# Kernel optimization log

Measured on AMD Instinct MI355X. Metric: run time of the kernel, lower is better.

## Reference

```python
import jax, jax.numpy as jnp
import numpy as np

B, N, E = 8, 50000, 800000
IN_DIM, OUT_DIM = 64, 64


def setup_inputs() -> dict:
    key = jax.random.key(0)
    k_x, k_src, k_dst, k_ws, k_bs, k_wn, k_bn = jax.random.split(key, 7)
    x = jax.random.normal(k_x, (B, N, IN_DIM), dtype=jnp.float32)
    src = jax.random.randint(k_src, (E,), 0, N, dtype=jnp.int64)
    dst = jax.random.randint(k_dst, (E,), 0, N, dtype=jnp.int64)
    edge_index = jnp.stack([src, dst], axis=1)  # (E, 2)
    # nn.Linear init: U(-1/sqrt(in_dim), 1/sqrt(in_dim))
    bound = 1.0 / np.sqrt(IN_DIM)
    W_self = jax.random.uniform(k_ws, (OUT_DIM, IN_DIM), jnp.float32, -bound, bound)
    b_self = jax.random.uniform(k_bs, (OUT_DIM,), jnp.float32, -bound, bound)
    W_neigh = jax.random.uniform(k_wn, (OUT_DIM, IN_DIM), jnp.float32, -bound, bound)
    b_neigh = jax.random.uniform(k_bn, (OUT_DIM,), jnp.float32, -bound, bound)
    return {"x": x, "edge_index": edge_index, "W_self": W_self, "b_self": b_self,
            "W_neigh": W_neigh, "b_neigh": b_neigh}


def reference(x, edge_index, W_self, b_self, W_neigh, b_neigh):
    # x: (B, N, D); edge_index: (E, 2) [src, dst], shared topology across batch
    src = edge_index[:, 0]
    dst = edge_index[:, 1]
    # scatter-add neighbor aggregation, vectorized over batch
    agg = jnp.zeros_like(x).at[:, dst].add(x[:, src])  # (B, N, D)
    h_self = jnp.einsum('bnd,od->bno', x, W_self) + b_self
    h_neigh = jnp.einsum('bnd,od->bno', agg, W_neigh) + b_neigh
    return jax.nn.relu(h_self + h_neigh)
```

## Files before the change

kernel.cpp:

```cpp
#include <hip/hip_runtime.h>

#define Bn 8
#define Nn 50000
#define En 800000
#define Dd 64
#define CAP 64

typedef __attribute__((ext_vector_type(8))) unsigned short ushort8;
typedef __attribute__((ext_vector_type(8))) __bf16 bf16x8;
typedef __attribute__((ext_vector_type(4))) float floatx4;

__device__ __forceinline__ unsigned short f2bf(float f) {
  unsigned int u = __builtin_bit_cast(unsigned int, f);
  u = (u + 0x7FFFu + ((u >> 16) & 1u)) >> 16;
  return (unsigned short)u;
}

__device__ __forceinline__ int swz(int row, int byte_in_row) {
  return (row * 256 + byte_in_row) ^ ((row & 7) << 4);
}

__global__ __launch_bounds__(256) void k_fconv(const float* __restrict__ x,
                                               unsigned short* __restrict__ xb,
                                               const int* __restrict__ ei,
                                               int* __restrict__ deg,
                                               unsigned short* __restrict__ bucket,
                                               const float* __restrict__ Ws,
                                               const float* __restrict__ Wn,
                                               const float* __restrict__ bs,
                                               const float* __restrict__ bn,
                                               unsigned short* __restrict__ Wb,
                                               float* __restrict__ bb) {
  const size_t gid = (size_t)blockIdx.x * 256 + threadIdx.x;
  const size_t i = gid * 4;
  const float4 v = *(const float4*)(x + i);
  ushort4 o;
  o.x = f2bf(v.x); o.y = f2bf(v.y); o.z = f2bf(v.z); o.w = f2bf(v.w);
  *(ushort4*)(xb + i) = o;
  if ((gid & 7) == 0) {
    const size_t e = gid >> 3;
    const int2 ep = *(const int2*)(ei + 2 * e);
    const int p = atomicAdd(&deg[ep.y], 1);
    if (p < CAP) bucket[((size_t)ep.y << 6) + p] = (unsigned short)ep.x;
  }
  if (gid < 1024) {
    const int f = (int)gid >> 6, ln = (int)gid & 63;
    const int t = f >> 2, k = f & 3;
    const int col = ln & 15, quad = ln >> 4;
    const int orow = t * 16 + col;
    const int kd = k * 32 + quad * 8;
    const float* wsrc = (kd < 64) ? (Ws + orow * 64 + kd) : (Wn + orow * 64 + (kd - 64));
    ushort8 u;
    #pragma unroll
    for (int j = 0; j < 8; ++j) u[j] = f2bf(wsrc[j]);
    *(ushort8*)(Wb + gid * 8) = u;
  }
  if (gid < 64) bb[gid] = bs[gid] + bn[gid];
}

__global__ __launch_bounds__(256, 8) void k_main(
    const unsigned short* __restrict__ xb, const unsigned short* __restrict__ bucket,
    const int* __restrict__ deg, const unsigned short* __restrict__ Wb,
    const float* __restrict__ bb, float* __restrict__ out) {
  __shared__ __align__(16) unsigned short A[64 * 128];

  const int tid = threadIdx.x;
  const int b = blockIdx.x & 7;
  const int node0 = (blockIdx.x >> 3) * 64;
  const int wave = tid >> 6;
  const int lane = tid & 63;
  char* Ac = (char*)A;

  const int slot = lane >> 3;
  const int li = lane & 7;
  const size_t xb_base = (size_t)b * Nn * Dd + (size_t)(li * 8);

  for (int g = 0; g < 2; ++g) {
    const int nl = wave * 16 + g * 8 + slot;
    const int node = node0 + nl;
    float acc[8] = {0.f, 0.f, 0.f, 0.f, 0.f, 0.f, 0.f, 0.f};
    if (node < Nn) {
      const uint4 sv = *(const uint4*)(xb + xb_base + (size_t)node * Dd);
      const int cnt = min(deg[node], CAP);
      const unsigned short* bkt = bucket + (node << 6);
      const int nch = (cnt + 7) >> 3;
      for (int c = 0; c < nch; ++c) {
        const uint4 e = *(const uint4*)(bkt + c * 8);
        const unsigned int ew[4] = {e.x, e.y, e.z, e.w};
        #pragma unroll
        for (int t = 0; t < 8; ++t) {
          unsigned int s = (ew[t >> 1] >> ((t & 1) * 16)) & 0xFFFFu;
          const float m = (s < (unsigned)Nn) ? 1.0f : 0.0f;
          s = min(s, (unsigned)(Nn - 1));
          const uint4 v = *(const uint4*)(xb + xb_base + (size_t)s * Dd);
          const unsigned int w[4] = {v.x, v.y, v.z, v.w};
          #pragma unroll
          for (int j = 0; j < 4; ++j) {
            acc[2 * j]     = fmaf(m, __builtin_bit_cast(float, w[j] << 16), acc[2 * j]);
            acc[2 * j + 1] = fmaf(m, __builtin_bit_cast(float, w[j] & 0xFFFF0000u), acc[2 * j + 1]);
          }
        }
      }
      *(uint4*)(Ac + swz(nl, li * 16)) = sv;
    } else {
      *(uint4*)(Ac + swz(nl, li * 16)) = make_uint4(0, 0, 0, 0);
    }
    ushort8 av;
    #pragma unroll
    for (int j = 0; j < 8; ++j) av[j] = f2bf(acc[j]);
    *(ushort8*)(Ac + swz(nl, 128 + li * 16)) = av;
  }

  const int col = lane & 15;
  const int quad = lane >> 4;
  bf16x8 af[4];
  {
    const int row = wave * 16 + col;
    #pragma unroll
    for (int k = 0; k < 4; ++k)
      af[k] = __builtin_bit_cast(bf16x8, *(const ushort8*)(Ac + swz(row, quad * 16 + k * 64)));
  }
  #pragma unroll
  for (int t = 0; t < 4; ++t) {
    floatx4 acc = {0.f, 0.f, 0.f, 0.f};
    #pragma unroll
    for (int k = 0; k < 4; ++k) {
      bf16x8 bf = __builtin_bit_cast(bf16x8, *(const ushort8*)(Wb + ((t * 4 + k) * 64 + lane) * 8));
      acc = __builtin_amdgcn_mfma_f32_16x16x32_bf16(af[k], bf, acc, 0, 0, 0);
    }
    const float bv = bb[t * 16 + col];
    #pragma unroll
    for (int r = 0; r < 4; ++r) {
      const int node = node0 + wave * 16 + quad * 4 + r;
      if (node < Nn) {
        float v = acc[r] + bv;
        out[((size_t)b * Nn + node) * Dd + t * 16 + col] = v > 0.f ? v : 0.f;
      }
    }
  }
}

#define OFF_XB 0ull
#define OFF_DEG 51200000ull
#define OFF_BKT 51400000ull
#define OFF_WB 57800000ull
#define OFF_BB 57816384ull
#define WS_NEED 57816640ull

extern "C" void kernel_launch(void* const* d_in, const int* in_sizes, int n_in,
                              void* d_out, int out_size, void* d_ws,
                              size_t ws_size, hipStream_t stream) {
  const float* x = (const float*)d_in[0];
  const int* ei = (const int*)d_in[1];
  const float* Ws = (const float*)d_in[2];
  const float* bs = (const float*)d_in[3];
  const float* Wn = (const float*)d_in[4];
  const float* bn = (const float*)d_in[5];
  float* out = (float*)d_out;

  if (ws_size < WS_NEED) return;

  char* ws = (char*)d_ws;
  unsigned short* xb = (unsigned short*)(ws + OFF_XB);
  int* deg = (int*)(ws + OFF_DEG);
  unsigned short* bucket = (unsigned short*)(ws + OFF_BKT);
  unsigned short* Wb = (unsigned short*)(ws + OFF_WB);
  float* bb = (float*)(ws + OFF_BB);

  hipMemsetAsync(deg, 0, Nn * sizeof(int), stream);
  hipMemsetAsync(bucket, 0xFF, (size_t)Nn * CAP * sizeof(unsigned short), stream);
  k_fconv<<<(Bn * Nn * Dd / 4) / 256, 256, 0, stream>>>(x, xb, ei, deg, bucket, Ws, Wn, bs, bn, Wb, bb);
  const int ntiles = (Nn + 63) / 64;
  k_main<<<ntiles * Bn, 256, 0, stream>>>(xb, bucket, deg, Wb, bb, out);
}
```

Before: 344.2 us.

## Interleave two nodes' gathers with batched loads and drop bucket memset

The gather loop now processes both nodes a thread owns together, issuing 16 independent row loads before accumulating and prefetching the next bucket chunk, so more memory requests are in flight per thread. Validity is now taken from the per-node count instead of a sentinel value, which makes the 6.4MB bucket memset unnecessary, so it is removed. Launch bounds drop from 8 to 3 blocks per SM to give room for the larger register footprint. The cost is lower occupancy, and both nodes run for the larger of their two chunk counts.

```diff
diff --git a/kernel.cpp b/kernel.cpp
--- a/kernel.cpp
+++ b/kernel.cpp
@@ -58,7 +58,7 @@
   if (gid < 64) bb[gid] = bs[gid] + bn[gid];
 }
 
-__global__ __launch_bounds__(256, 8) void k_main(
+__global__ __launch_bounds__(256, 3) void k_main(
     const unsigned short* __restrict__ xb, const unsigned short* __restrict__ bucket,
     const int* __restrict__ deg, const unsigned short* __restrict__ Wb,
     const float* __restrict__ bb, float* __restrict__ out) {
@@ -75,41 +75,89 @@
   const int li = lane & 7;
   const size_t xb_base = (size_t)b * Nn * Dd + (size_t)(li * 8);
 
-  for (int g = 0; g < 2; ++g) {
-    const int nl = wave * 16 + g * 8 + slot;
-    const int node = node0 + nl;
-    float acc[8] = {0.f, 0.f, 0.f, 0.f, 0.f, 0.f, 0.f, 0.f};
-    if (node < Nn) {
-      const uint4 sv = *(const uint4*)(xb + xb_base + (size_t)node * Dd);
-      const int cnt = min(deg[node], CAP);
-      const unsigned short* bkt = bucket + (node << 6);
-      const int nch = (cnt + 7) >> 3;
-      for (int c = 0; c < nch; ++c) {
-        const uint4 e = *(const uint4*)(bkt + c * 8);
-        const unsigned int ew[4] = {e.x, e.y, e.z, e.w};
-        #pragma unroll
-        for (int t = 0; t < 8; ++t) {
-          unsigned int s = (ew[t >> 1] >> ((t & 1) * 16)) & 0xFFFFu;
-          const float m = (s < (unsigned)Nn) ? 1.0f : 0.0f;
-          s = min(s, (unsigned)(Nn - 1));
-          const uint4 v = *(const uint4*)(xb + xb_base + (size_t)s * Dd);
-          const unsigned int w[4] = {v.x, v.y, v.z, v.w};
-          #pragma unroll
-          for (int j = 0; j < 4; ++j) {
-            acc[2 * j]     = fmaf(m, __builtin_bit_cast(float, w[j] << 16), acc[2 * j]);
-            acc[2 * j + 1] = fmaf(m, __builtin_bit_cast(float, w[j] & 0xFFFF0000u), acc[2 * j + 1]);
-          }
-        }
+  const int nl0 = wave * 16 + slot;
+  const int nl1 = nl0 + 8;
+  const int n0 = node0 + nl0;
+  const int n1 = node0 + nl1;
+  const bool v0 = n0 < Nn, v1 = n1 < Nn;
+  const int n0c = v0 ? n0 : 0, n1c = v1 ? n1 : 0;
+
+  const int cnt0 = v0 ? min(deg[n0c], CAP) : 0;
+  const int cnt1 = v1 ? min(deg[n1c], CAP) : 0;
+  const unsigned short* bkt0 = bucket + ((size_t)n0c << 6);
+  const unsigned short* bkt1 = bucket + ((size_t)n1c << 6);
+
+  uint4 sv0 = *(const uint4*)(xb + xb_base + (size_t)n0c * Dd);
+  uint4 sv1 = *(const uint4*)(xb + xb_base + (size_t)n1c * Dd);
+
+  const int nch0 = (cnt0 + 7) >> 3;
+  const int nch1 = (cnt1 + 7) >> 3;
+  const int nch = max(nch0, nch1);
+
+  float a0[8] = {0.f, 0.f, 0.f, 0.f, 0.f, 0.f, 0.f, 0.f};
+  float a1[8] = {0.f, 0.f, 0.f, 0.f, 0.f, 0.f, 0.f, 0.f};
+
+  uint4 e0 = make_uint4(0, 0, 0, 0), e1 = e0;
+  if (nch > 0) {
+    e0 = *(const uint4*)(bkt0);
+    e1 = *(const uint4*)(bkt1);
+  }
+  for (int c = 0; c < nch; ++c) {
+    uint4 ne0 = e0, ne1 = e1;
+    if (c + 1 < nch) {
+      ne0 = *(const uint4*)(bkt0 + (c + 1) * 8);
+      ne1 = *(const uint4*)(bkt1 + (c + 1) * 8);
+    }
+    const unsigned int ew0[4] = {e0.x, e0.y, e0.z, e0.w};
+    const unsigned int ew1[4] = {e1.x, e1.y, e1.z, e1.w};
+    uint4 g0[8], g1[8];
+    float m0[8], m1[8];
+    #pragma unroll
+    for (int t = 0; t < 8; ++t) {
+      unsigned int s = (ew0[t >> 1] >> ((t & 1) * 16)) & 0xFFFFu;
+      const bool live = (c * 8 + t) < cnt0;
+      m0[t] = live ? 1.0f : 0.0f;
+      s = live ? min(s, (unsigned)(Nn - 1)) : (unsigned)(Nn - 1);
+      g0[t] = *(const uint4*)(xb + xb_base + (size_t)s * Dd);
+    }
+    #pragma unroll
+    for (int t = 0; t < 8; ++t) {
+      unsigned int s = (ew1[t >> 1] >> ((t & 1) * 16)) & 0xFFFFu;
+      const bool live = (c * 8 + t) < cnt1;
+      m1[t] = live ? 1.0f : 0.0f;
+      s = live ? min(s, (unsigned)(Nn - 1)) : (unsigned)(Nn - 1);
+      g1[t] = *(const uint4*)(xb + xb_base + (size_t)s * Dd);
+    }
+    #pragma unroll
+    for (int t = 0; t < 8; ++t) {
+      const unsigned int* w = (const unsigned int*)&g0[t];
+      #pragma unroll
+      for (int j = 0; j < 4; ++j) {
+        a0[2 * j]     = fmaf(m0[t], __builtin_bit_cast(float, w[j] << 16), a0[2 * j]);
+        a0[2 * j + 1] = fmaf(m0[t], __builtin_bit_cast(float, w[j] & 0xFFFF0000u), a0[2 * j + 1]);
       }
-      *(uint4*)(Ac + swz(nl, li * 16)) = sv;
-    } else {
-      *(uint4*)(Ac + swz(nl, li * 16)) = make_uint4(0, 0, 0, 0);
-    }
-    ushort8 av;
-    #pragma unroll
-    for (int j = 0; j < 8; ++j) av[j] = f2bf(acc[j]);
-    *(ushort8*)(Ac + swz(nl, 128 + li * 16)) = av;
-  }
+    }
+    #pragma unroll
+    for (int t = 0; t < 8; ++t) {
+      const unsigned int* w = (const unsigned int*)&g1[t];
+      #pragma unroll
+      for (int j = 0; j < 4; ++j) {
+        a1[2 * j]     = fmaf(m1[t], __builtin_bit_cast(float, w[j] << 16), a1[2 * j]);
+        a1[2 * j + 1] = fmaf(m1[t], __builtin_bit_cast(float, w[j] & 0xFFFF0000u), a1[2 * j + 1]);
+      }
+    }
+    e0 = ne0; e1 = ne1;
+  }
+
+  if (!v0) sv0 = make_uint4(0, 0, 0, 0);
+  if (!v1) sv1 = make_uint4(0, 0, 0, 0);
+  *(uint4*)(Ac + swz(nl0, li * 16)) = sv0;
+  *(uint4*)(Ac + swz(nl1, li * 16)) = sv1;
+  ushort8 av0, av1;
+  #pragma unroll
+  for (int j = 0; j < 8; ++j) { av0[j] = f2bf(a0[j]); av1[j] = f2bf(a1[j]); }
+  *(ushort8*)(Ac + swz(nl0, 128 + li * 16)) = av0;
+  *(ushort8*)(Ac + swz(nl1, 128 + li * 16)) = av1;
 
   const int col = lane & 15;
   const int quad = lane >> 4;
@@ -168,7 +216,6 @@
   float* bb = (float*)(ws + OFF_BB);
 
   hipMemsetAsync(deg, 0, Nn * sizeof(int), stream);
-  hipMemsetAsync(bucket, 0xFF, (size_t)Nn * CAP * sizeof(unsigned short), stream);
   k_fconv<<<(Bn * Nn * Dd / 4) / 256, 256, 0, stream>>>(x, xb, ei, deg, bucket, Ws, Wn, bs, bn, Wb, bb);
   const int ntiles = (Nn + 63) / 64;
   k_main<<<ntiles * Bn, 256, 0, stream>>>(xb, bucket, deg, Wb, bb, out);
```

Result: faster. 319.1 us (-7.3%).

## Interleave batch into node-major bf16 layout so each gather serves all batches

Applied to the files above, without the earlier changes.

The bf16 copy of x is now stored node-major with the 8 batches interleaved, giving each node 512 contiguous elements. One wave lane-group gathers a neighbour's row for all batches in a single 1 KB contiguous access, and the bucket indices are read once per node instead of once per batch. The main kernel now handles 16 nodes times 8 batches per block, prefetches the next index chunk, issues all 8 gathers before accumulating, masks by count instead of a sentinel, and uses nontemporal loads and stores. The bucket memset is dropped, and the 1024 weight-prep threads in the conversion kernel now run alongside 2x-wide conversion threads. Occupancy drops because of the larger LDS tile and the launch bound change from 8 to 4 blocks.

```diff
diff --git a/kernel.cpp b/kernel.cpp
--- a/kernel.cpp
+++ b/kernel.cpp
@@ -9,6 +9,7 @@
 typedef __attribute__((ext_vector_type(8))) unsigned short ushort8;
 typedef __attribute__((ext_vector_type(8))) __bf16 bf16x8;
 typedef __attribute__((ext_vector_type(4))) float floatx4;
+typedef __attribute__((ext_vector_type(2))) int intx2;
 
 __device__ __forceinline__ unsigned short f2bf(float f) {
   unsigned int u = __builtin_bit_cast(unsigned int, f);
@@ -32,16 +33,22 @@
                                                unsigned short* __restrict__ Wb,
                                                float* __restrict__ bb) {
   const size_t gid = (size_t)blockIdx.x * 256 + threadIdx.x;
-  const size_t i = gid * 4;
-  const float4 v = *(const float4*)(x + i);
-  ushort4 o;
-  o.x = f2bf(v.x); o.y = f2bf(v.y); o.z = f2bf(v.z); o.w = f2bf(v.w);
-  *(ushort4*)(xb + i) = o;
-  if ((gid & 7) == 0) {
-    const size_t e = gid >> 3;
-    const int2 ep = *(const int2*)(ei + 2 * e);
+  const size_t i = gid * 8;
+  const floatx4 v0 = __builtin_nontemporal_load((const floatx4*)(x + i));
+  const floatx4 v1 = __builtin_nontemporal_load((const floatx4*)(x + i + 4));
+  ushort8 o;
+  o[0] = f2bf(v0.x); o[1] = f2bf(v0.y); o[2] = f2bf(v0.z); o[3] = f2bf(v0.w);
+  o[4] = f2bf(v1.x); o[5] = f2bf(v1.y); o[6] = f2bf(v1.z); o[7] = f2bf(v1.w);
+  const unsigned int b = (unsigned int)(i / (Nn * (size_t)Dd));
+  const unsigned int r = (unsigned int)(i - (size_t)b * (Nn * Dd));
+  const unsigned int n = r >> 6, d = r & 63;
+  *(ushort8*)(xb + (size_t)n * 512 + b * 64 + d) = o;
+  if ((gid & 3) == 0) {
+    const size_t e = gid >> 2;
+    const intx2 ep = __builtin_nontemporal_load((const intx2*)(ei + 2 * e));
     const int p = atomicAdd(&deg[ep.y], 1);
-    if (p < CAP) bucket[((size_t)ep.y << 6) + p] = (unsigned short)ep.x;
+    if (p < CAP)
+      __builtin_nontemporal_store((unsigned short)ep.x, &bucket[((size_t)ep.y << 6) + p]);
   }
   if (gid < 1024) {
     const int f = (int)gid >> 6, ln = (int)gid & 63;
@@ -58,83 +65,101 @@
   if (gid < 64) bb[gid] = bs[gid] + bn[gid];
 }
 
-__global__ __launch_bounds__(256, 8) void k_main(
+__global__ __launch_bounds__(256, 4) void k_main(
     const unsigned short* __restrict__ xb, const unsigned short* __restrict__ bucket,
     const int* __restrict__ deg, const unsigned short* __restrict__ Wb,
     const float* __restrict__ bb, float* __restrict__ out) {
-  __shared__ __align__(16) unsigned short A[64 * 128];
+  __shared__ __align__(16) unsigned short A[128 * 128];
 
   const int tid = threadIdx.x;
-  const int b = blockIdx.x & 7;
-  const int node0 = (blockIdx.x >> 3) * 64;
-  const int wave = tid >> 6;
   const int lane = tid & 63;
+  const int wave = __builtin_amdgcn_readfirstlane(tid >> 6);
+  const int node0 = blockIdx.x * 16;
   char* Ac = (char*)A;
+  const int lofs = lane * 8;
 
-  const int slot = lane >> 3;
-  const int li = lane & 7;
-  const size_t xb_base = (size_t)b * Nn * Dd + (size_t)(li * 8);
+  uint4 selfq[4], idx0[4];
+  int cntq[4];
+  #pragma unroll
+  for (int q = 0; q < 4; ++q) {
+    const int node = node0 + wave * 4 + q;
+    cntq[q] = min(deg[node], CAP);
+    selfq[q] = *(const uint4*)(xb + (size_t)node * 512 + lofs);
+    idx0[q] = *(const uint4*)(bucket + ((size_t)node << 6));
+  }
+  #pragma unroll
+  for (int q = 0; q < 4; ++q) {
+    const int row = (wave * 4 + q) * 8 + (lane >> 3);
+    *(uint4*)(Ac + swz(row, (lane & 7) * 16)) = selfq[q];
+  }
 
-  for (int g = 0; g < 2; ++g) {
-    const int nl = wave * 16 + g * 8 + slot;
-    const int node = node0 + nl;
+  for (int q = 0; q < 4; ++q) {
+    const int node = node0 + wave * 4 + q;
+    const int cnt = cntq[q];
+    const unsigned short* bkt = bucket + ((size_t)node << 6);
+    const int nch = (cnt + 7) >> 3;
     float acc[8] = {0.f, 0.f, 0.f, 0.f, 0.f, 0.f, 0.f, 0.f};
-    if (node < Nn) {
-      const uint4 sv = *(const uint4*)(xb + xb_base + (size_t)node * Dd);
-      const int cnt = min(deg[node], CAP);
-      const unsigned short* bkt = bucket + (node << 6);
-      const int nch = (cnt + 7) >> 3;
-      for (int c = 0; c < nch; ++c) {
-        const uint4 e = *(const uint4*)(bkt + c * 8);
-        const unsigned int ew[4] = {e.x, e.y, e.z, e.w};
+    uint4 e = idx0[q];
+    for (int c = 0; c < nch; ++c) {
+      uint4 ne = e;
+      if (c + 1 < nch) ne = *(const uint4*)(bkt + (c + 1) * 8);
+      const unsigned int ew[4] = {e.x, e.y, e.z, e.w};
+      uint4 g[8];
+      float m[8];
+      #pragma unroll
+      for (int t = 0; t < 8; ++t) {
+        unsigned int s = (ew[t >> 1] >> ((t & 1) * 16)) & 0xFFFFu;
+        const bool live = (c * 8 + t) < cnt;
+        m[t] = live ? 1.0f : 0.0f;
+        s = live ? s : (unsigned)(Nn - 1);
+        g[t] = *(const uint4*)(xb + (size_t)s * 512 + lofs);
+      }
+      #pragma unroll
+      for (int t = 0; t < 8; ++t) {
+        const unsigned int* w = (const unsigned int*)&g[t];
         #pragma unroll
-        for (int t = 0; t < 8; ++t) {
-          unsigned int s = (ew[t >> 1] >> ((t & 1) * 16)) & 0xFFFFu;
-          const float m = (s < (unsigned)Nn) ? 1.0f : 0.0f;
-          s = min(s, (unsigned)(Nn - 1));
-          const uint4 v = *(const uint4*)(xb + xb_base + (size_t)s * Dd);
-          const unsigned int w[4] = {v.x, v.y, v.z, v.w};
-          #pragma unroll
-          for (int j = 0; j < 4; ++j) {
-            acc[2 * j]     = fmaf(m, __builtin_bit_cast(float, w[j] << 16), acc[2 * j]);
-            acc[2 * j + 1] = fmaf(m, __builtin_bit_cast(float, w[j] & 0xFFFF0000u), acc[2 * j + 1]);
-          }
+        for (int j = 0; j < 4; ++j) {
+          acc[2 * j]     = fmaf(m[t], __builtin_bit_cast(float, w[j] << 16), acc[2 * j]);
+          acc[2 * j + 1] = fmaf(m[t], __builtin_bit_cast(float, w[j] & 0xFFFF0000u), acc[2 * j + 1]);
         }
       }
-      *(uint4*)(Ac + swz(nl, li * 16)) = sv;
-    } else {
-      *(uint4*)(Ac + swz(nl, li * 16)) = make_uint4(0, 0, 0, 0);
+      e = ne;
     }
     ushort8 av;
     #pragma unroll
     for (int j = 0; j < 8; ++j) av[j] = f2bf(acc[j]);
-    *(ushort8*)(Ac + swz(nl, 128 + li * 16)) = av;
+    const int row = (wave * 4 + q) * 8 + (lane >> 3);
+    *(ushort8*)(Ac + swz(row, 128 + (lane & 7) * 16)) = av;
   }
 
   const int col = lane & 15;
   const int quad = lane >> 4;
-  bf16x8 af[4];
-  {
-    const int row = wave * 16 + col;
+  #pragma unroll
+  for (int mi = 0; mi < 2; ++mi) {
+    const int mt = wave * 2 + mi;
+    bf16x8 af[4];
+    {
+      const int row = mt * 16 + col;
+      #pragma unroll
+      for (int k = 0; k < 4; ++k)
+        af[k] = __builtin_bit_cast(bf16x8, *(const ushort8*)(Ac + swz(row, k * 64 + quad * 16)));
+    }
     #pragma unroll
-    for (int k = 0; k < 4; ++k)
-      af[k] = __builtin_bit_cast(bf16x8, *(const ushort8*)(Ac + swz(row, quad * 16 + k * 64)));
-  }
-  #pragma unroll
-  for (int t = 0; t < 4; ++t) {
-    floatx4 acc = {0.f, 0.f, 0.f, 0.f};
-    #pragma unroll
-    for (int k = 0; k < 4; ++k) {
-      bf16x8 bf = __builtin_bit_cast(bf16x8, *(const ushort8*)(Wb + ((t * 4 + k) * 64 + lane) * 8));
-      acc = __builtin_amdgcn_mfma_f32_16x16x32_bf16(af[k], bf, acc, 0, 0, 0);
-    }
-    const float bv = bb[t * 16 + col];
-    #pragma unroll
-    for (int r = 0; r < 4; ++r) {
-      const int node = node0 + wave * 16 + quad * 4 + r;
-      if (node < Nn) {
-        float v = acc[r] + bv;
-        out[((size_t)b * Nn + node) * Dd + t * 16 + col] = v > 0.f ? v : 0.f;
+    for (int t = 0; t < 4; ++t) {
+      floatx4 acc = {0.f, 0.f, 0.f, 0.f};
+      #pragma unroll
+      for (int k = 0; k < 4; ++k) {
+        bf16x8 bf = __builtin_bit_cast(bf16x8, *(const ushort8*)(Wb + ((t * 4 + k) * 64 + lane) * 8));
+        acc = __builtin_amdgcn_mfma_f32_16x16x32_bf16(af[k], bf, acc, 0, 0, 0);
+      }
+      const float bv = bb[t * 16 + col];
+      #pragma unroll
+      for (int r = 0; r < 4; ++r) {
+        const int orow = mt * 16 + quad * 4 + r;
+        const int nl = orow >> 3, b = orow & 7;
+        const float v = acc[r] + bv;
+        __builtin_nontemporal_store(v > 0.f ? v : 0.f,
+                                    &out[((size_t)b * Nn + node0 + nl) * Dd + t * 16 + col]);
       }
     }
   }
@@ -168,8 +193,6 @@
   float* bb = (float*)(ws + OFF_BB);
 
   hipMemsetAsync(deg, 0, Nn * sizeof(int), stream);
-  hipMemsetAsync(bucket, 0xFF, (size_t)Nn * CAP * sizeof(unsigned short), stream);
-  k_fconv<<<(Bn * Nn * Dd / 4) / 256, 256, 0, stream>>>(x, xb, ei, deg, bucket, Ws, Wn, bs, bn, Wb, bb);
-  const int ntiles = (Nn + 63) / 64;
-  k_main<<<ntiles * Bn, 256, 0, stream>>>(xb, bucket, deg, Wb, bb, out);
+  k_fconv<<<(Bn * Nn * Dd / 8) / 256, 256, 0, stream>>>(x, xb, ei, deg, bucket, Ws, Wn, bs, bn, Wb, bb);
+  k_main<<<Nn / 16, 256, 0, stream>>>(xb, bucket, deg, Wb, bb, out);
 }
```

Result: faster. 333.0 us (-3.3%).
